# Optimization experiments

Measured on AMD Instinct MI355X. Metric: run time of the kernel, lower is better.

## Reference

```python
import jax, jax.numpy as jnp
import numpy as np

COMMITMENT_COST = 0.25
EPSILON = 1e-5


def setup_inputs() -> dict:
    key = jax.random.key(0)
    k1, k2, k3 = jax.random.split(key, 3)
    B, T, D, M = 64, 512, 256, 1024
    audio_semantic = jax.random.normal(k1, (B, T, D), dtype=jnp.float32)
    eeg_semantic = jax.random.normal(k2, (B, T, D), dtype=jnp.float32)
    init_bound = 1.0 / 400.0
    embedding = jax.random.uniform(k3, (M, D), dtype=jnp.float32,
                                   minval=-init_bound, maxval=init_bound)
    return {"audio_semantic": audio_semantic, "eeg_semantic": eeg_semantic,
            "embedding": embedding}


def _distances(flat, embedding):
    return (jnp.sum(embedding ** 2, axis=1)
            + jnp.sum(flat ** 2, axis=1, keepdims=True)
            - 2.0 * (flat @ embedding.T))


def reference(audio_semantic, eeg_semantic, embedding):
    M, D = embedding.shape
    B, T, _ = audio_semantic.shape
    N = B * T
    a_flat = audio_semantic.reshape(-1, D)
    e_flat = eeg_semantic.reshape(-1, D)

    a_dis = _distances(a_flat, embedding)  # [N, M]
    e_dis = _distances(e_flat, embedding)

    # soft assignment probabilities (clamp tiny negative dists before sqrt)
    a_ph = jax.nn.softmax(-jnp.sqrt(jnp.maximum(a_dis, 0.0)), axis=1)
    a_ph = a_ph.reshape(B, T, M).mean(axis=1)  # [B, M]
    e_ph = jax.nn.softmax(-jnp.sqrt(jnp.maximum(e_dis, 0.0)), axis=1)
    e_ph = e_ph.reshape(B, T, M).mean(axis=1)

    # cross-modal code matching loss
    Scode = a_ph @ jnp.log(e_ph.T + 1e-10) + e_ph @ jnp.log(a_ph.T + 1e-10)  # [B, B]
    MaxScode = jnp.max(-Scode)
    EScode = jnp.exp(Scode + MaxScode)
    Lcmcm = -jnp.mean(jnp.log(jnp.diag(EScode) / (jnp.sum(EScode, axis=1) + EPSILON)))
    cmcm_loss = 0.5 * Lcmcm

    # hard assignment + codebook gather
    a_indices = jnp.argmin(a_dis, axis=-1)  # [N]
    e_indices = jnp.argmin(e_dis, axis=-1)
    a_quantized = embedding[a_indices].reshape(B, T, D)
    e_quantized = embedding[e_indices].reshape(B, T, D)

    # per-sample mode of indices (ties -> smallest index, like torch.mode)
    a_counts = jax.nn.one_hot(a_indices.reshape(B, T), M, dtype=jnp.float32).sum(axis=1)
    e_counts = jax.nn.one_hot(e_indices.reshape(B, T), M, dtype=jnp.float32).sum(axis=1)
    a_mode = jnp.argmax(a_counts, axis=-1)
    e_mode = jnp.argmax(e_counts, axis=-1)
    equal_num = jnp.sum(a_mode == e_mode)

    # commitment losses (quantized detached)
    a_q_sg = jax.lax.stop_gradient(a_quantized)
    e_q_sg = jax.lax.stop_gradient(e_quantized)
    a_e_latent = jnp.mean((audio_semantic - a_q_sg) ** 2)
    ae_e_latent = jnp.mean((audio_semantic - e_q_sg) ** 2)
    a_loss = COMMITMENT_COST * (2.0 * a_e_latent + ae_e_latent)
    e_e_latent = jnp.mean((eeg_semantic - e_q_sg) ** 2)
    ea_e_latent = jnp.mean((eeg_semantic - a_q_sg) ** 2)
    e_loss = COMMITMENT_COST * (2.0 * e_e_latent + ea_e_latent)

    # straight-through estimator
    a_quantized_st = audio_semantic + jax.lax.stop_gradient(a_quantized - audio_semantic)
    e_quantized_st = eeg_semantic + jax.lax.stop_gradient(e_quantized - eeg_semantic)

    # perplexity from average usage
    a_avg = jnp.zeros((M,), jnp.float32).at[a_indices].add(1.0) / N
    e_avg = jnp.zeros((M,), jnp.float32).at[e_indices].add(1.0) / N
    a_perplexity = jnp.exp(-jnp.sum(a_avg * jnp.log(a_avg + 1e-10)))
    e_perplexity = jnp.exp(-jnp.sum(e_avg * jnp.log(e_avg + 1e-10)))

    return (a_quantized_st, e_quantized_st, a_loss, e_loss,
            a_perplexity, e_perplexity, cmcm_loss, equal_num)
```

## Files before the change

kernel.cpp:

```cpp
#include <hip/hip_runtime.h>
#include <math.h>

#define Bn 64
#define Tn 512
#define Dn 256
#define Mn 1024
#define Nn (Bn * Tn)
#define NnDn ((size_t)Nn * Dn)

typedef __attribute__((ext_vector_type(8))) short short8v;
typedef __attribute__((ext_vector_type(4))) float float4v;

#define OFF_APH   0
#define OFF_EPH   65536
#define OFF_ACNT  131072
#define OFF_ECNT  196608
#define OFF_LAT   262144
#define ZERO_FLOATS 262656
#define OFF_SE2   262656
#define OFF_EH    263680
#define OFF_EL    394752
#define OFF_APHN  525824
#define OFF_EPHN  591360
#define OFF_LA    656896
#define OFF_LE    722432
#define OFF_SCODE 787968
#define OUT_SCALARS ((size_t)2 * Nn * Dn)

__device__ __forceinline__ unsigned short bf16hi(float x) {
  unsigned u = __float_as_uint(x);
  return (unsigned short)((u + 0x7FFFu + ((u >> 16) & 1u)) >> 16);
}
__device__ __forceinline__ float bf16tof(unsigned short h) {
  return __uint_as_float(((unsigned)h) << 16);
}

__global__ __launch_bounds__(256) void kPrepE(const float* __restrict__ emb,
                                              float* __restrict__ ws) {
  unsigned short* Eh = (unsigned short*)(ws + OFF_EH);
  unsigned short* El = (unsigned short*)(ws + OFF_EL);
  float* se2 = ws + OFF_SE2;
  const int tid = threadIdx.x;
  const int row = blockIdx.x * 32 + (tid >> 3);
  const int sub = tid & 7;
  const float* src = emb + (size_t)row * Dn + sub * 32;
  unsigned short* dh = Eh + (size_t)row * Dn + sub * 32;
  unsigned short* dl = El + (size_t)row * Dn + sub * 32;
  float s2 = 0.f;
  for (int g = 0; g < 4; ++g) {
    float4 v0 = ((const float4*)src)[g * 2];
    float4 v1 = ((const float4*)src)[g * 2 + 1];
    float xs[8] = {v0.x, v0.y, v0.z, v0.w, v1.x, v1.y, v1.z, v1.w};
    short8v hv, lv;
    #pragma unroll
    for (int j = 0; j < 8; ++j) {
      s2 = fmaf(xs[j], xs[j], s2);
      unsigned short h = bf16hi(xs[j]);
      hv[j] = (short)h;
      lv[j] = (short)bf16hi(xs[j] - bf16tof(h));
    }
    *(short8v*)(dh + g * 8) = hv;
    *(short8v*)(dl + g * 8) = lv;
  }
  s2 += __shfl_xor(s2, 1); s2 += __shfl_xor(s2, 2); s2 += __shfl_xor(s2, 4);
  if (sub == 0) se2[row] = s2;
}

__global__ __launch_bounds__(512, 1) void kMain(
    const float* __restrict__ audio, const float* __restrict__ eeg,
    const float* __restrict__ emb, float* out, float* __restrict__ ws) {
  __shared__ unsigned short Xh[64 * 128];
  __shared__ unsigned short Xl[64 * 128];
  __shared__ float se2l[Mn];
  __shared__ float sx2l[64];
  __shared__ float wmin[64][8];
  __shared__ int   widx[64][8];
  __shared__ float wZ[64][8];
  __shared__ float rowLs[64];
  __shared__ int   rowIdxs[64];
  __shared__ float izs[64];
  __shared__ float redm[8][4];

  const int tid = threadIdx.x;
  const int n0 = blockIdx.x * 32;
  const int b = blockIdx.x >> 4;
  const unsigned short* Eh = (const unsigned short*)(ws + OFF_EH);
  const unsigned short* El = (const unsigned short*)(ws + OFF_EL);

  const int lane = tid & 63, wid = tid >> 6;
  const int c = lane & 15, g = lane >> 4;
  const int colbase = wid * 128;

  se2l[tid] = ws[OFF_SE2 + tid];
  se2l[tid + 512] = ws[OFF_SE2 + tid + 512];

  float4v acc[4][8];
  #pragma unroll
  for (int rg = 0; rg < 4; ++rg)
    #pragma unroll
    for (int cg = 0; cg < 8; ++cg) {
      float4v z = {0.f, 0.f, 0.f, 0.f};
      acc[rg][cg] = z;
    }

  const int srow = tid >> 3, ssub = tid & 7;
  const float* ssrc = (srow < 32) ? (audio + (size_t)(n0 + srow) * Dn)
                                  : (eeg + (size_t)(n0 + srow - 32) * Dn);
  const int sswz = (srow & 7) << 4;
  char* XhB = (char*)Xh;
  char* XlB = (char*)Xl;
  int rowb[4], swzr[4];
  #pragma unroll
  for (int rg = 0; rg < 4; ++rg) {
    int row = rg * 16 + c;
    rowb[rg] = row * 256;
    swzr[rg] = (row & 7) << 4;
  }
  int eoff[8];
  #pragma unroll
  for (int cg = 0; cg < 8; ++cg)
    eoff[cg] = (colbase + cg * 16 + c) * 256 + g * 8;

  float s2 = 0.f;
  for (int ph = 0; ph < 2; ++ph) {
    if (ph) __syncthreads();
    {
      const int d0 = ssub * 16;
      const float* sp = ssrc + ph * 128 + d0;
      #pragma unroll
      for (int g2 = 0; g2 < 2; ++g2) {
        float4 v0 = ((const float4*)sp)[g2 * 2];
        float4 v1 = ((const float4*)sp)[g2 * 2 + 1];
        float xs[8] = {v0.x, v0.y, v0.z, v0.w, v1.x, v1.y, v1.z, v1.w};
        short8v hv, lv;
        #pragma unroll
        for (int j = 0; j < 8; ++j) {
          s2 = fmaf(xs[j], xs[j], s2);
          unsigned short h = bf16hi(xs[j]);
          hv[j] = (short)h;
          lv[j] = (short)bf16hi(xs[j] - bf16tof(h));
        }
        const int ab = (srow * 256 + (d0 + g2 * 8) * 2) ^ sswz;
        *(short8v*)(XhB + ab) = hv;
        *(short8v*)(XlB + ab) = lv;
      }
    }
    __syncthreads();
    for (int ks4 = 0; ks4 < 4; ++ks4) {
      const int kb = ks4 * 64 + g * 16;
      const int kg = ph * 128 + ks4 * 32;
      short8v ah[4], al[4];
      #pragma unroll
      for (int rg = 0; rg < 4; ++rg) {
        const int ab = rowb[rg] + (kb ^ swzr[rg]);
        ah[rg] = *(const short8v*)(XhB + ab);
        al[rg] = *(const short8v*)(XlB + ab);
      }
      #pragma unroll
      for (int cg = 0; cg < 8; ++cg) {
        short8v bh = *(const short8v*)(Eh + eoff[cg] + kg);
        short8v bl = *(const short8v*)(El + eoff[cg] + kg);
        #pragma unroll
        for (int rg = 0; rg < 4; ++rg) {
          acc[rg][cg] = __builtin_amdgcn_mfma_f32_16x16x32_bf16(ah[rg], bh, acc[rg][cg], 0, 0, 0);
          acc[rg][cg] = __builtin_amdgcn_mfma_f32_16x16x32_bf16(al[rg], bh, acc[rg][cg], 0, 0, 0);
          acc[rg][cg] = __builtin_amdgcn_mfma_f32_16x16x32_bf16(ah[rg], bl, acc[rg][cg], 0, 0, 0);
        }
      }
    }
  }
  s2 += __shfl_xor(s2, 1); s2 += __shfl_xor(s2, 2); s2 += __shfl_xor(s2, 4);
  if (ssub == 0) sx2l[srow] = s2;

  float se2c[8];
  #pragma unroll
  for (int cg = 0; cg < 8; ++cg) se2c[cg] = se2l[colbase + cg * 16 + c];
  #pragma unroll
  for (int rg = 0; rg < 4; ++rg)
    #pragma unroll
    for (int cg = 0; cg < 8; ++cg)
      #pragma unroll
      for (int q = 0; q < 4; ++q)
        acc[rg][cg][q] = fmaf(-2.f, acc[rg][cg][q], se2c[cg]);

  float vmin[4][4]; int imin[4][4];
  #pragma unroll
  for (int rg = 0; rg < 4; ++rg)
    #pragma unroll
    for (int q = 0; q < 4; ++q) { vmin[rg][q] = 3.0e38f; imin[rg][q] = Mn; }
  #pragma unroll
  for (int cg = 0; cg < 8; ++cg) {
    const int colc = colbase + cg * 16 + c;
    #pragma unroll
    for (int rg = 0; rg < 4; ++rg)
      #pragma unroll
      for (int q = 0; q < 4; ++q) {
        float v = acc[rg][cg][q];
        if (v < vmin[rg][q]) { vmin[rg][q] = v; imin[rg][q] = colc; }
      }
  }
  #pragma unroll
  for (int off = 1; off <= 8; off <<= 1) {
    #pragma unroll
    for (int rg = 0; rg < 4; ++rg)
      #pragma unroll
      for (int q = 0; q < 4; ++q) {
        float ov = __shfl_xor(vmin[rg][q], off);
        int oi = __shfl_xor(imin[rg][q], off);
        if (ov < vmin[rg][q] || (ov == vmin[rg][q] && oi < imin[rg][q])) {
          vmin[rg][q] = ov; imin[rg][q] = oi;
        }
      }
  }
  if (c == 0) {
    #pragma unroll
    for (int rg = 0; rg < 4; ++rg)
      #pragma unroll
      for (int q = 0; q < 4; ++q) {
        int row = rg * 16 + g * 4 + q;
        wmin[row][wid] = vmin[rg][q];
        widx[row][wid] = imin[rg][q];
      }
  }
  __syncthreads();
  if (tid < 64) {
    float m = wmin[tid][0]; int mi = widx[tid][0];
    #pragma unroll
    for (int w = 1; w < 8; ++w) {
      float v = wmin[tid][w]; int i2 = widx[tid][w];
      if (v < m || (v == m && i2 < mi)) { m = v; mi = i2; }
    }
    rowIdxs[tid] = mi;
    rowLs[tid] = sqrtf(fmaxf(m + sx2l[tid], 0.f));
  }
  __syncthreads();
  if (tid < 32) atomicAdd((unsigned*)(ws + OFF_ACNT) + b * Mn + rowIdxs[tid], 1u);
  else if (tid < 64) atomicAdd((unsigned*)(ws + OFF_ECNT) + b * Mn + rowIdxs[tid], 1u);

  float Lpre[4][4], spre[4][4];
  #pragma unroll
  for (int rg = 0; rg < 4; ++rg)
    #pragma unroll
    for (int q = 0; q < 4; ++q) {
      int row = rg * 16 + g * 4 + q;
      Lpre[rg][q] = rowLs[row];
      spre[rg][q] = sx2l[row];
    }
  float zp[4][4];
  #pragma unroll
  for (int rg = 0; rg < 4; ++rg)
    #pragma unroll
    for (int q = 0; q < 4; ++q) zp[rg][q] = 0.f;
  #pragma unroll
  for (int rg = 0; rg < 4; ++rg)
    #pragma unroll
    for (int cg = 0; cg < 8; ++cg)
      #pragma unroll
      for (int q = 0; q < 4; ++q) {
        float d = acc[rg][cg][q] + spre[rg][q];
        float pv = __expf(Lpre[rg][q] - sqrtf(fmaxf(d, 0.f)));
        acc[rg][cg][q] = pv;
        zp[rg][q] += pv;
      }
  #pragma unroll
  for (int off = 1; off <= 8; off <<= 1)
    #pragma unroll
    for (int rg = 0; rg < 4; ++rg)
      #pragma unroll
      for (int q = 0; q < 4; ++q) zp[rg][q] += __shfl_xor(zp[rg][q], off);
  if (c == 0) {
    #pragma unroll
    for (int rg = 0; rg < 4; ++rg)
      #pragma unroll
      for (int q = 0; q < 4; ++q) wZ[rg * 16 + g * 4 + q][wid] = zp[rg][q];
  }
  __syncthreads();
  if (tid < 64) {
    float Z = 0.f;
    #pragma unroll
    for (int w = 0; w < 8; ++w) Z += wZ[tid][w];
    izs[tid] = 1.f / Z;
  }
  __syncthreads();

  float izq[4][4];
  #pragma unroll
  for (int rg = 0; rg < 4; ++rg)
    #pragma unroll
    for (int q = 0; q < 4; ++q) izq[rg][q] = izs[rg * 16 + g * 4 + q];
  float psA[8], psE[8];
  #pragma unroll
  for (int cg = 0; cg < 8; ++cg) {
    float a = 0.f, e = 0.f;
    #pragma unroll
    for (int q = 0; q < 4; ++q) {
      a += acc[0][cg][q] * izq[0][q] + acc[1][cg][q] * izq[1][q];
      e += acc[2][cg][q] * izq[2][q] + acc[3][cg][q] * izq[3][q];
    }
    a += __shfl_xor(a, 16); a += __shfl_xor(a, 32);
    e += __shfl_xor(e, 16); e += __shfl_xor(e, 32);
    psA[cg] = a; psE[cg] = e;
  }
  if (lane < 16) {
    float* phA = ws + OFF_APH;
    float* phE = ws + OFF_EPH;
    #pragma unroll
    for (int cg = 0; cg < 8; ++cg) {
      int colc = colbase + cg * 16 + lane;
      atomicAdd(phA + b * Mn + colc, psA[cg]);
      atomicAdd(phE + b * Mn + colc, psE[cg]);
    }
  }

  {
    const int r = tid >> 4, pp = tid & 15;
    const int ia = rowIdxs[r], ie = rowIdxs[32 + r];
    const float4* qa = (const float4*)(emb + (size_t)ia * Dn);
    const float4* qe = (const float4*)(emb + (size_t)ie * Dn);
    const float4* xa4 = (const float4*)(audio + (size_t)(n0 + r) * Dn);
    const float4* xe4 = (const float4*)(eeg + (size_t)(n0 + r) * Dn);
    float4* oA = (float4*)(out + (size_t)(n0 + r) * Dn);
    float4* oE = (float4*)(out + NnDn + (size_t)(n0 + r) * Dn);
    float s_ae = 0.f, s_aq = 0.f, s_ee = 0.f, s_eq = 0.f;
    #pragma unroll
    for (int h = 0; h < 4; ++h) {
      const int i4 = pp * 4 + h;
      float4 qav = qa[i4], qev = qe[i4], xav = xa4[i4], xev = xe4[i4];
      float qaf[4] = {qav.x, qav.y, qav.z, qav.w};
      float qef[4] = {qev.x, qev.y, qev.z, qev.w};
      float xaf[4] = {xav.x, xav.y, xav.z, xav.w};
      float xef[4] = {xev.x, xev.y, xev.z, xev.w};
      #pragma unroll
      for (int j = 0; j < 4; ++j) {
        float d1 = xaf[j] - qaf[j]; s_ae += d1 * d1;
        float d2 = xaf[j] - qef[j]; s_aq += d2 * d2;
        float d3 = xef[j] - qef[j]; s_ee += d3 * d3;
        float d4 = xef[j] - qaf[j]; s_eq += d4 * d4;
      }
      oA[i4] = qav;
      oE[i4] = qev;
    }
    #pragma unroll
    for (int off = 1; off <= 32; off <<= 1) {
      s_ae += __shfl_xor(s_ae, off);
      s_aq += __shfl_xor(s_aq, off);
      s_ee += __shfl_xor(s_ee, off);
      s_eq += __shfl_xor(s_eq, off);
    }
    if (lane == 0) {
      redm[wid][0] = s_ae; redm[wid][1] = s_aq;
      redm[wid][2] = s_ee; redm[wid][3] = s_eq;
    }
    __syncthreads();
    if (tid < 4) {
      float t = 0.f;
      #pragma unroll
      for (int w = 0; w < 8; ++w) t += redm[w][tid];
      atomicAdd(ws + OFF_LAT + tid, t);
    }
  }
}

__global__ __launch_bounds__(256) void kC0(float* __restrict__ ws) {
  int i = blockIdx.x * 256 + threadIdx.x;
  float a = ws[OFF_APH + i] * (1.f / 512.f);
  float e = ws[OFF_EPH + i] * (1.f / 512.f);
  ws[OFF_APHN + i] = a;
  ws[OFF_EPHN + i] = e;
  ws[OFF_LA + i] = logf(a + 1e-10f);
  ws[OFF_LE + i] = logf(e + 1e-10f);
}

__global__ __launch_bounds__(256) void kC1(float* __restrict__ ws) {
  const int i = blockIdx.x;
  const int tid = threadIdx.x;
  const int j = tid >> 2, q = tid & 3;
  const float* ai  = ws + OFF_APHN + (size_t)i * Mn;
  const float* ei  = ws + OFF_EPHN + (size_t)i * Mn;
  const float* lej = ws + OFF_LE + (size_t)j * Mn;
  const float* laj = ws + OFF_LA + (size_t)j * Mn;
  float s = 0.f;
  for (int m = q * 256; m < (q + 1) * 256; ++m)
    s += ai[m] * lej[m] + ei[m] * laj[m];
  s += __shfl_xor(s, 1);
  s += __shfl_xor(s, 2);
  if (q == 0) ws[OFF_SCODE + i * 64 + j] = s;
}

__global__ __launch_bounds__(256) void kC2(float* __restrict__ ws, float* __restrict__ out) {
  __shared__ float sc[4096];
  __shared__ float red[256];
  __shared__ float rterm[64];
  __shared__ float maxv;
  const int tid = threadIdx.x;
  const float* scode = ws + OFF_SCODE;
  for (int i = tid; i < 4096; i += 256) sc[i] = scode[i];
  __syncthreads();

  float mx = -3.0e38f;
  for (int i = tid; i < 4096; i += 256) mx = fmaxf(mx, -sc[i]);
  red[tid] = mx; __syncthreads();
  for (int s = 128; s > 0; s >>= 1) {
    if (tid < s) red[tid] = fmaxf(red[tid], red[tid + s]);
    __syncthreads();
  }
  if (tid == 0) maxv = red[0];
  __syncthreads();
  const float Max = maxv;

  if (tid < 64) {
    float rs = 0.f;
    for (int j = 0; j < 64; ++j) rs += expf(sc[tid * 64 + j] + Max);
    float dg = expf(sc[tid * 64 + tid] + Max);
    rterm[tid] = logf(dg / (rs + 1e-5f));
  }
  __syncthreads();
  if (tid == 0) {
    float s = 0.f;
    for (int i = 0; i < 64; ++i) s += rterm[i];
    out[OUT_SCALARS + 4] = -0.5f * s / 64.f;
  }
  if (tid == 1) {
    const float* lat = ws + OFF_LAT;
    const float inv = 1.f / 8388608.f;
    float a_e = lat[0] * inv, ae = lat[1] * inv, e_e = lat[2] * inv, ea = lat[3] * inv;
    out[OUT_SCALARS + 0] = 0.25f * (2.f * a_e + ae);
    out[OUT_SCALARS + 1] = 0.25f * (2.f * e_e + ea);
  }

  const unsigned* acnt = (const unsigned*)(ws + OFF_ACNT);
  const unsigned* ecnt = (const unsigned*)(ws + OFF_ECNT);
  float enta = 0.f, ente = 0.f;
  for (int mm = tid; mm < Mn; mm += 256) {
    unsigned ta = 0, te = 0;
    for (int bb = 0; bb < Bn; ++bb) { ta += acnt[bb * Mn + mm]; te += ecnt[bb * Mn + mm]; }
    float av = (float)ta * (1.f / 32768.f);
    float ev = (float)te * (1.f / 32768.f);
    enta += av * logf(av + 1e-10f);
    ente += ev * logf(ev + 1e-10f);
  }
  __syncthreads(); red[tid] = enta; __syncthreads();
  for (int s = 128; s > 0; s >>= 1) { if (tid < s) red[tid] += red[tid + s]; __syncthreads(); }
  if (tid == 0) out[OUT_SCALARS + 2] = expf(-red[0]);
  __syncthreads(); red[tid] = ente; __syncthreads();
  for (int s = 128; s > 0; s >>= 1) { if (tid < s) red[tid] += red[tid + s]; __syncthreads(); }
  if (tid == 0) out[OUT_SCALARS + 3] = expf(-red[0]);

  {
    int row = tid >> 2, qq = tid & 3;
    unsigned bA = 0; int ia = qq * 256;
    unsigned bE = 0; int ie = qq * 256;
    for (int m = qq * 256; m < qq * 256 + 256; ++m) {
      unsigned ca = acnt[row * Mn + m]; if (ca > bA) { bA = ca; ia = m; }
      unsigned ce = ecnt[row * Mn + m]; if (ce > bE) { bE = ce; ie = m; }
    }
    #pragma unroll
    for (int off = 1; off <= 2; off <<= 1) {
      unsigned ob = (unsigned)__shfl_xor((int)bA, off); int oi = __shfl_xor(ia, off);
      if (ob > bA || (ob == bA && oi < ia)) { bA = ob; ia = oi; }
      unsigned oe = (unsigned)__shfl_xor((int)bE, off); int oj = __shfl_xor(ie, off);
      if (oe > bE || (oe == bE && oj < ie)) { bE = oe; ie = oj; }
    }
    float eq = (qq == 0 && ia == ie) ? 1.f : 0.f;
    __syncthreads(); red[tid] = eq; __syncthreads();
    for (int s = 128; s > 0; s >>= 1) { if (tid < s) red[tid] += red[tid + s]; __syncthreads(); }
    if (tid == 0) out[OUT_SCALARS + 5] = red[0];
  }
}

extern "C" void kernel_launch(void* const* d_in, const int* in_sizes, int n_in,
                              void* d_out, int out_size, void* d_ws, size_t ws_size,
                              hipStream_t stream) {
  const float* audio = (const float*)d_in[0];
  const float* eeg   = (const float*)d_in[1];
  const float* emb   = (const float*)d_in[2];
  float* out = (float*)d_out;
  float* ws  = (float*)d_ws;
  (void)in_sizes; (void)n_in; (void)out_size; (void)ws_size;

  hipMemsetAsync(d_ws, 0, (size_t)ZERO_FLOATS * sizeof(float), stream);
  hipLaunchKernelGGL(kPrepE, dim3(32), dim3(256), 0, stream, emb, ws);
  hipLaunchKernelGGL(kMain, dim3(Nn / 32), dim3(512), 0, stream, audio, eeg, emb, out, ws);
  hipLaunchKernelGGL(kC0, dim3(256), dim3(256), 0, stream, ws);
  hipLaunchKernelGGL(kC1, dim3(64), dim3(256), 0, stream, ws);
  hipLaunchKernelGGL(kC2, dim3(1), dim3(256), 0, stream, ws, out);
}
```

Baseline: 402.9 us.

## Re-layout bf16 codebook by k-chunk, allow two blocks per CU, parallelize tail kernels

```diff
diff --git a/kernel.cpp b/kernel.cpp
--- a/kernel.cpp
+++ b/kernel.cpp
@@ -16,6 +16,9 @@
 #define OFF_ACNT  131072
 #define OFF_ECNT  196608
 #define OFF_LAT   262144
+#define OFF_ENT   262148
+#define OFF_MODEA 262152
+#define OFF_MODEE 262216
 #define ZERO_FLOATS 262656
 #define OFF_SE2   262656
 #define OFF_EH    263680
@@ -41,15 +44,16 @@
   unsigned short* El = (unsigned short*)(ws + OFF_EL);
   float* se2 = ws + OFF_SE2;
   const int tid = threadIdx.x;
-  const int row = blockIdx.x * 32 + (tid >> 3);
+  const int m = blockIdx.x * 32 + (tid >> 3);
   const int sub = tid & 7;
-  const float* src = emb + (size_t)row * Dn + sub * 32;
-  unsigned short* dh = Eh + (size_t)row * Dn + sub * 32;
-  unsigned short* dl = El + (size_t)row * Dn + sub * 32;
+  const float* src = emb + (size_t)m * Dn + sub * 32;
+  unsigned short* dh = Eh + (size_t)sub * 32768 + m * 32;
+  unsigned short* dl = El + (size_t)sub * 32768 + m * 32;
   float s2 = 0.f;
-  for (int g = 0; g < 4; ++g) {
-    float4 v0 = ((const float4*)src)[g * 2];
-    float4 v1 = ((const float4*)src)[g * 2 + 1];
+  #pragma unroll
+  for (int gq = 0; gq < 4; ++gq) {
+    float4 v0 = ((const float4*)src)[gq * 2];
+    float4 v1 = ((const float4*)src)[gq * 2 + 1];
     float xs[8] = {v0.x, v0.y, v0.z, v0.w, v1.x, v1.y, v1.z, v1.w};
     short8v hv, lv;
     #pragma unroll
@@ -59,14 +63,14 @@
       hv[j] = (short)h;
       lv[j] = (short)bf16hi(xs[j] - bf16tof(h));
     }
-    *(short8v*)(dh + g * 8) = hv;
-    *(short8v*)(dl + g * 8) = lv;
+    *(short8v*)(dh + gq * 8) = hv;
+    *(short8v*)(dl + gq * 8) = lv;
   }
   s2 += __shfl_xor(s2, 1); s2 += __shfl_xor(s2, 2); s2 += __shfl_xor(s2, 4);
-  if (sub == 0) se2[row] = s2;
-}
-
-__global__ __launch_bounds__(512, 1) void kMain(
+  if (sub == 0) se2[m] = s2;
+}
+
+__global__ __launch_bounds__(512, 2) void kMain(
     const float* __restrict__ audio, const float* __restrict__ eeg,
     const float* __restrict__ emb, float* out, float* __restrict__ ws) {
   __shared__ unsigned short Xh[64 * 128];
@@ -84,8 +88,8 @@
   const int tid = threadIdx.x;
   const int n0 = blockIdx.x * 32;
   const int b = blockIdx.x >> 4;
-  const unsigned short* Eh = (const unsigned short*)(ws + OFF_EH);
-  const unsigned short* El = (const unsigned short*)(ws + OFF_EL);
+  const unsigned short* __restrict__ Eh = (const unsigned short*)(ws + OFF_EH);
+  const unsigned short* __restrict__ El = (const unsigned short*)(ws + OFF_EL);
 
   const int lane = tid & 63, wid = tid >> 6;
   const int c = lane & 15, g = lane >> 4;
@@ -116,10 +120,7 @@
     rowb[rg] = row * 256;
     swzr[rg] = (row & 7) << 4;
   }
-  int eoff[8];
-  #pragma unroll
-  for (int cg = 0; cg < 8; ++cg)
-    eoff[cg] = (colbase + cg * 16 + c) * 256 + g * 8;
+  const int eoffv = c * 32 + g * 8;
 
   float s2 = 0.f;
   for (int ph = 0; ph < 2; ++ph) {
@@ -148,7 +149,10 @@
     __syncthreads();
     for (int ks4 = 0; ks4 < 4; ++ks4) {
       const int kb = ks4 * 64 + g * 16;
-      const int kg = ph * 128 + ks4 * 32;
+      const unsigned short* peh = Eh + (size_t)(ph * 4 + ks4) * 32768
+                                     + (size_t)colbase * 32 + eoffv;
+      const unsigned short* pel = El + (size_t)(ph * 4 + ks4) * 32768
+                                     + (size_t)colbase * 32 + eoffv;
       short8v ah[4], al[4];
       #pragma unroll
       for (int rg = 0; rg < 4; ++rg) {
@@ -158,8 +162,8 @@
       }
       #pragma unroll
       for (int cg = 0; cg < 8; ++cg) {
-        short8v bh = *(const short8v*)(Eh + eoff[cg] + kg);
-        short8v bl = *(const short8v*)(El + eoff[cg] + kg);
+        short8v bh = *(const short8v*)(peh + cg * 512);
+        short8v bl = *(const short8v*)(pel + cg * 512);
         #pragma unroll
         for (int rg = 0; rg < 4; ++rg) {
           acc[rg][cg] = __builtin_amdgcn_mfma_f32_16x16x32_bf16(ah[rg], bh, acc[rg][cg], 0, 0, 0);
@@ -372,29 +376,87 @@
 }
 
 __global__ __launch_bounds__(256) void kC1(float* __restrict__ ws) {
-  const int i = blockIdx.x;
-  const int tid = threadIdx.x;
-  const int j = tid >> 2, q = tid & 3;
+  const int blk = blockIdx.x;
+  const int i = blk >> 2, jq = blk & 3;
+  const int t = threadIdx.x;
+  const int jj = t >> 4, q = t & 15;
+  const int j = jq * 16 + jj;
   const float* ai  = ws + OFF_APHN + (size_t)i * Mn;
   const float* ei  = ws + OFF_EPHN + (size_t)i * Mn;
   const float* lej = ws + OFF_LE + (size_t)j * Mn;
   const float* laj = ws + OFF_LA + (size_t)j * Mn;
   float s = 0.f;
-  for (int m = q * 256; m < (q + 1) * 256; ++m)
+  #pragma unroll 4
+  for (int m = q * 64; m < q * 64 + 64; ++m)
     s += ai[m] * lej[m] + ei[m] * laj[m];
-  s += __shfl_xor(s, 1);
-  s += __shfl_xor(s, 2);
+  s += __shfl_xor(s, 1); s += __shfl_xor(s, 2);
+  s += __shfl_xor(s, 4); s += __shfl_xor(s, 8);
   if (q == 0) ws[OFF_SCODE + i * 64 + j] = s;
 }
 
-__global__ __launch_bounds__(256) void kC2(float* __restrict__ ws, float* __restrict__ out) {
+__global__ __launch_bounds__(256) void kMode(float* __restrict__ ws) {
+  const int bb = blockIdx.x;
+  const unsigned* acnt = (const unsigned*)(ws + OFF_ACNT) + (size_t)bb * Mn;
+  const unsigned* ecnt = (const unsigned*)(ws + OFF_ECNT) + (size_t)bb * Mn;
+  __shared__ unsigned rv[256]; __shared__ int ri[256];
+  __shared__ unsigned rv2[256]; __shared__ int ri2[256];
+  const int t = threadIdx.x;
+  unsigned bA = 0; int ia = t;
+  unsigned bE = 0; int ie = t;
+  #pragma unroll
+  for (int m = t; m < Mn; m += 256) {
+    unsigned ca = acnt[m]; if (ca > bA) { bA = ca; ia = m; }
+    unsigned ce = ecnt[m]; if (ce > bE) { bE = ce; ie = m; }
+  }
+  rv[t] = bA; ri[t] = ia; rv2[t] = bE; ri2[t] = ie;
+  __syncthreads();
+  for (int s2 = 128; s2 > 0; s2 >>= 1) {
+    if (t < s2) {
+      if (rv[t + s2] > rv[t] || (rv[t + s2] == rv[t] && ri[t + s2] < ri[t])) {
+        rv[t] = rv[t + s2]; ri[t] = ri[t + s2];
+      }
+      if (rv2[t + s2] > rv2[t] || (rv2[t + s2] == rv2[t] && ri2[t + s2] < ri2[t])) {
+        rv2[t] = rv2[t + s2]; ri2[t] = ri2[t + s2];
+      }
+    }
+    __syncthreads();
+  }
+  if (t == 0) {
+    ((int*)ws)[OFF_MODEA + bb] = ri[0];
+    ((int*)ws)[OFF_MODEE + bb] = ri2[0];
+  }
+}
+
+__global__ __launch_bounds__(128) void kPerp(float* __restrict__ ws) {
+  const int t = threadIdx.x;
+  const int m = blockIdx.x * 128 + t;
+  const unsigned* acnt = (const unsigned*)(ws + OFF_ACNT);
+  const unsigned* ecnt = (const unsigned*)(ws + OFF_ECNT);
+  unsigned ta = 0, te = 0;
+  for (int bb = 0; bb < Bn; ++bb) { ta += acnt[(size_t)bb * Mn + m]; te += ecnt[(size_t)bb * Mn + m]; }
+  float av = (float)ta * (1.f / 32768.f);
+  float ev = (float)te * (1.f / 32768.f);
+  float ea = av * logf(av + 1e-10f);
+  float ee = ev * logf(ev + 1e-10f);
+  #pragma unroll
+  for (int off = 1; off <= 32; off <<= 1) { ea += __shfl_xor(ea, off); ee += __shfl_xor(ee, off); }
+  __shared__ float r[2][2];
+  const int lane = t & 63, w = t >> 6;
+  if (lane == 0) { r[w][0] = ea; r[w][1] = ee; }
+  __syncthreads();
+  if (t == 0) {
+    atomicAdd(ws + OFF_ENT + 0, r[0][0] + r[1][0]);
+    atomicAdd(ws + OFF_ENT + 1, r[0][1] + r[1][1]);
+  }
+}
+
+__global__ __launch_bounds__(256) void kFin(float* __restrict__ ws, float* __restrict__ out) {
   __shared__ float sc[4096];
   __shared__ float red[256];
   __shared__ float rterm[64];
   __shared__ float maxv;
   const int tid = threadIdx.x;
-  const float* scode = ws + OFF_SCODE;
-  for (int i = tid; i < 4096; i += 256) sc[i] = scode[i];
+  for (int i = tid; i < 4096; i += 256) sc[i] = ws[OFF_SCODE + i];
   __syncthreads();
 
   float mx = -3.0e38f;
@@ -427,44 +489,14 @@
     out[OUT_SCALARS + 0] = 0.25f * (2.f * a_e + ae);
     out[OUT_SCALARS + 1] = 0.25f * (2.f * e_e + ea);
   }
-
-  const unsigned* acnt = (const unsigned*)(ws + OFF_ACNT);
-  const unsigned* ecnt = (const unsigned*)(ws + OFF_ECNT);
-  float enta = 0.f, ente = 0.f;
-  for (int mm = tid; mm < Mn; mm += 256) {
-    unsigned ta = 0, te = 0;
-    for (int bb = 0; bb < Bn; ++bb) { ta += acnt[bb * Mn + mm]; te += ecnt[bb * Mn + mm]; }
-    float av = (float)ta * (1.f / 32768.f);
-    float ev = (float)te * (1.f / 32768.f);
-    enta += av * logf(av + 1e-10f);
-    ente += ev * logf(ev + 1e-10f);
-  }
-  __syncthreads(); red[tid] = enta; __syncthreads();
-  for (int s = 128; s > 0; s >>= 1) { if (tid < s) red[tid] += red[tid + s]; __syncthreads(); }
-  if (tid == 0) out[OUT_SCALARS + 2] = expf(-red[0]);
-  __syncthreads(); red[tid] = ente; __syncthreads();
-  for (int s = 128; s > 0; s >>= 1) { if (tid < s) red[tid] += red[tid + s]; __syncthreads(); }
-  if (tid == 0) out[OUT_SCALARS + 3] = expf(-red[0]);
-
-  {
-    int row = tid >> 2, qq = tid & 3;
-    unsigned bA = 0; int ia = qq * 256;
-    unsigned bE = 0; int ie = qq * 256;
-    for (int m = qq * 256; m < qq * 256 + 256; ++m) {
-      unsigned ca = acnt[row * Mn + m]; if (ca > bA) { bA = ca; ia = m; }
-      unsigned ce = ecnt[row * Mn + m]; if (ce > bE) { bE = ce; ie = m; }
-    }
-    #pragma unroll
-    for (int off = 1; off <= 2; off <<= 1) {
-      unsigned ob = (unsigned)__shfl_xor((int)bA, off); int oi = __shfl_xor(ia, off);
-      if (ob > bA || (ob == bA && oi < ia)) { bA = ob; ia = oi; }
-      unsigned oe = (unsigned)__shfl_xor((int)bE, off); int oj = __shfl_xor(ie, off);
-      if (oe > bE || (oe == bE && oj < ie)) { bE = oe; ie = oj; }
-    }
-    float eq = (qq == 0 && ia == ie) ? 1.f : 0.f;
-    __syncthreads(); red[tid] = eq; __syncthreads();
-    for (int s = 128; s > 0; s >>= 1) { if (tid < s) red[tid] += red[tid + s]; __syncthreads(); }
-    if (tid == 0) out[OUT_SCALARS + 5] = red[0];
+  if (tid == 2) out[OUT_SCALARS + 2] = expf(-ws[OFF_ENT + 0]);
+  if (tid == 3) out[OUT_SCALARS + 3] = expf(-ws[OFF_ENT + 1]);
+  if (tid == 4) {
+    const int* ma = (const int*)ws + OFF_MODEA;
+    const int* me = (const int*)ws + OFF_MODEE;
+    int eq = 0;
+    for (int b2 = 0; b2 < 64; ++b2) eq += (ma[b2] == me[b2]) ? 1 : 0;
+    out[OUT_SCALARS + 5] = (float)eq;
   }
 }
 
@@ -482,6 +514,8 @@
   hipLaunchKernelGGL(kPrepE, dim3(32), dim3(256), 0, stream, emb, ws);
   hipLaunchKernelGGL(kMain, dim3(Nn / 32), dim3(512), 0, stream, audio, eeg, emb, out, ws);
   hipLaunchKernelGGL(kC0, dim3(256), dim3(256), 0, stream, ws);
-  hipLaunchKernelGGL(kC1, dim3(64), dim3(256), 0, stream, ws);
-  hipLaunchKernelGGL(kC2, dim3(1), dim3(256), 0, stream, ws, out);
-}
+  hipLaunchKernelGGL(kC1, dim3(256), dim3(256), 0, stream, ws);
+  hipLaunchKernelGGL(kMode, dim3(64), dim3(256), 0, stream, ws);
+  hipLaunchKernelGGL(kPerp, dim3(8), dim3(128), 0, stream, ws);
+  hipLaunchKernelGGL(kFin, dim3(1), dim3(256), 0, stream, ws, out);
+}
```

New measurement: 339.5 us. -15.7%, faster.
